# Optimization experiments

Hardware: AMD Instinct MI355X
Metric: run time of the kernel (lower is better)

The kernel has to match this reference:

```python
import jax, jax.numpy as jnp
import numpy as np

N = 100000      # nodes
E = 3200000     # edges (avg degree 32)
F_IN = 16       # data.num_features
H = 16          # hidden width (hard-coded in module)
C = 2           # data.num_classes
N_MID = 5       # conv2..conv6


def setup_inputs() -> dict:
    key = jax.random.key(0)
    ks = jax.random.split(key, 12)
    s = lambda fan_in: 1.0 / np.sqrt(fan_in)
    x = jax.random.normal(ks[0], (N, F_IN), jnp.float32)
    edge_index = jax.random.randint(ks[1], (2, E), 0, N, jnp.int32)
    return {
        "x": x,
        "edge_index": edge_index,
        "Wl1": jax.random.normal(ks[2], (F_IN, H), jnp.float32) * s(F_IN),
        "Wr1": jax.random.normal(ks[3], (F_IN, H), jnp.float32) * s(F_IN),
        "b1": jnp.zeros((H,), jnp.float32),
        "Wl_mid": jax.random.normal(ks[4], (N_MID, H, H), jnp.float32) * s(H),
        "Wr_mid": jax.random.normal(ks[5], (N_MID, H, H), jnp.float32) * s(H),
        "b_mid": jnp.zeros((N_MID, H), jnp.float32),
        "Wl7": jax.random.normal(ks[6], (H, C), jnp.float32) * s(H),
        "Wr7": jax.random.normal(ks[7], (H, C), jnp.float32) * s(H),
        "b7": jnp.zeros((C,), jnp.float32),
    }


def _sage_conv(x, src, dst, Wl, bl, Wr):
    # PyG SAGEConv(aggr='max'): out = lin_l(max_j x_j) + lin_r(x_i)
    msg = x[src]                                  # [E, F] neighbor gather
    agg = jax.ops.segment_max(msg, dst, num_segments=N)
    agg = jnp.where(jnp.isfinite(agg), agg, 0.0)  # isolated nodes -> 0
    return agg @ Wl + bl + x @ Wr


def reference(x, edge_index, Wl1, Wr1, b1, Wl_mid, Wr_mid, b_mid, Wl7, Wr7, b7):
    src, dst = edge_index[0], edge_index[1]
    h = jax.nn.relu(_sage_conv(x, src, dst, Wl1, b1, Wr1))
    for i in range(N_MID):
        h = jax.nn.relu(_sage_conv(h, src, dst, Wl_mid[i], b_mid[i], Wr_mid[i]))
    # F.dropout with training=False (inference) is identity
    h = _sage_conv(h, src, dst, Wl7, b7, Wr7)
    return jax.nn.log_softmax(h, axis=1)
```

## Files before the change

### kernel.cpp

```cpp
#include <hip/hip_runtime.h>
#include <hip/hip_fp16.h>

#define N_NODES 100000
#define N_EDGES 3200000
#define HDIM 16
#define NB 391
#define PAIRCAP 9216
#define COLCAP 13312
#define P1_THREADS 512
#define P1_EPB 4096
#define P1_BLOCKS ((N_EDGES + P1_EPB - 1) / P1_EPB)
#define SENT 0xFBFFFBFFu

typedef unsigned u32;

__device__ __forceinline__ u32 pkmax(u32 a, u32 b) {
    u32 r;
    asm("v_pk_max_f16 %0, %1, %2" : "=v"(r) : "v"(a), "v"(b));
    return r;
}
__device__ __forceinline__ float2 h2f2(u32 u) {
    __half2 h = *reinterpret_cast<__half2*>(&u);
    return __half22float2(h);
}
__device__ __forceinline__ u32 f2h2(float a, float b) {
    __half2 h = __float22half2_rn(make_float2(a, b));
    return *reinterpret_cast<u32*>(&h);
}


__global__ void f2h_zero(const float4* __restrict__ x, uint2* __restrict__ o, int n,
                         int* __restrict__ gcur) {
    int t = threadIdx.x;
    if (blockIdx.x == 0) {
        for (int k = t; k < NB; k += blockDim.x) gcur[k] = 0;
    }
    if (blockIdx.x == 1 && t < 8) {
        ((u32*)o)[(size_t)N_NODES * 8 + t] = SENT;
    }
    int i = blockIdx.x * blockDim.x + t;
    if (i < n) {
        float4 v = x[i];
        o[i] = make_uint2(f2h2(v.x, v.y), f2h2(v.z, v.w));
    }
}


__global__ __launch_bounds__(P1_THREADS)
void pass1_bucket(const int* __restrict__ src, const int* __restrict__ dst,
                  int* __restrict__ gcur, unsigned* __restrict__ pairs) {
    __shared__ int lh[NB], lbase[NB];
    int t = threadIdx.x;
    int e0 = blockIdx.x * P1_EPB;
    int n = min(P1_EPB, N_EDGES - e0);
    for (int i = t; i < NB; i += P1_THREADS) lh[i] = 0;
    __syncthreads();
    unsigned pv[8];
    int bk[8], rr[8];
#pragma unroll
    for (int k = 0; k < 8; ++k) {
        int idx = k * P1_THREADS + t;
        if (idx < n) {
            int d = dst[e0 + idx];
            int s = src[e0 + idx];
            bk[k] = d >> 8;
            pv[k] = (unsigned)s | ((unsigned)(d & 255) << 17);
            rr[k] = atomicAdd(&lh[bk[k]], 1);
        }
    }
    __syncthreads();
    for (int i = t; i < NB; i += P1_THREADS) {
        int c = lh[i];
        lbase[i] = c ? atomicAdd(&gcur[i], c) : 0;
    }
    __syncthreads();
#pragma unroll
    for (int k = 0; k < 8; ++k) {
        int idx = k * P1_THREADS + t;
        if (idx < n) {
            int p = lbase[bk[k]] + rr[k];
            if (p < PAIRCAP)
                pairs[(size_t)bk[k] * COLCAP + p] = pv[k];
        }
    }
}


__global__ __launch_bounds__(1024)
void pass2_sort(unsigned* __restrict__ colbuf, const int* __restrict__ gcur,
                int2* __restrict__ row2) {
    __shared__ int sdeg[256], spd[256], ssc[256];
    __shared__ int colst[COLCAP];
    __shared__ int stot;
    int t = threadIdx.x;
    int b = blockIdx.x;
    size_t base = (size_t)b * COLCAP;
    int cnt = min(gcur[b], PAIRCAP);
    int node0 = b << 8;
    int nn = min(256, N_NODES - node0);
    if (t < 256) sdeg[t] = 0;
    __syncthreads();
    unsigned vv[9];
    int rr[9];
#pragma unroll
    for (int k = 0; k < 9; ++k) {
        int j = k * 1024 + t;
        if (j < cnt) {
            unsigned v = colbuf[base + j];
            vv[k] = v;
            rr[k] = atomicAdd(&sdeg[v >> 17], 1);
        }
    }
    __syncthreads();
    if (t < 256) {
        int d = sdeg[t];
        int pd = (d + 15) & ~15;
        spd[t] = pd;
        ssc[t] = pd;
    }
    __syncthreads();
    for (int off = 1; off < 256; off <<= 1) {
        int u = 0;
        if (t < 256 && t >= off) u = ssc[t - off];
        __syncthreads();
        if (t < 256) ssc[t] += u;
        __syncthreads();
    }
    if (t < 256) {
        int ex = ssc[t] - spd[t];
        ssc[t] = ex;
        if (t < nn) row2[node0 + t] = make_int2((int)base + ex, (int)base + ex + spd[t]);
        if (t == 255) stot = ex + spd[t];
        for (int q = ex + sdeg[t]; q < ex + spd[t]; ++q)
            colst[q] = N_NODES;
    }
    __syncthreads();
#pragma unroll
    for (int k = 0; k < 9; ++k) {
        int j = k * 1024 + t;
        if (j < cnt) {
            unsigned v = vv[k];
            colst[ssc[v >> 17] + rr[k]] = v & 0x1FFFF;
        }
    }
    __syncthreads();
    int tot = stot;
    for (int j = t; j < tot; j += 1024) colbuf[base + j] = (unsigned)colst[j];
}


template <int HOUT, bool RELU, bool LSM>
__global__ void sage_layer(const u32* __restrict__ h,
                           const int2* __restrict__ row2,
                           const unsigned* __restrict__ col,
                           const float* __restrict__ Wl,
                           const float* __restrict__ Wr,
                           const float* __restrict__ b,
                           void* __restrict__ out) {
    __shared__ float sWl[HDIM * HOUT];
    __shared__ float sWr[HDIM * HOUT];
    __shared__ float sb[HOUT];
    int t = threadIdx.x;
    if (t < HDIM * HOUT) { sWl[t] = Wl[t]; sWr[t] = Wr[t]; }
    if (t < HOUT) sb[t] = b[t];
    if (HOUT == 16) {
        if (blockIdx.x == 0 && t < 8)
            ((u32*)out)[(size_t)N_NODES * 8 + t] = SENT;
    }
    __syncthreads();

    int nl = t >> 3, g = t & 7, p = g >> 1, hf = g & 1;
    int i = blockIdx.x * 32 + nl;
    if (i >= N_NODES) return;

    int2 r2 = row2[i];
    int beg = r2.x, endp = r2.y;
    const uint4* h4 = (const uint4*)h;

    u32 a0 = SENT, a1 = SENT, a2 = SENT, a3 = SENT;
    for (int j = beg; j < endp; j += 16) {
        int n0 = (int)col[j + p];
        int n1 = (int)col[j + 4 + p];
        int n2 = (int)col[j + 8 + p];
        int n3 = (int)col[j + 12 + p];
        uint4 v0 = h4[n0 * 2 + hf];
        uint4 v1 = h4[n1 * 2 + hf];
        uint4 v2 = h4[n2 * 2 + hf];
        uint4 v3 = h4[n3 * 2 + hf];
        a0 = pkmax(a0, pkmax(pkmax(v0.x, v1.x), pkmax(v2.x, v3.x)));
        a1 = pkmax(a1, pkmax(pkmax(v0.y, v1.y), pkmax(v2.y, v3.y)));
        a2 = pkmax(a2, pkmax(pkmax(v0.z, v1.z), pkmax(v2.z, v3.z)));
        a3 = pkmax(a3, pkmax(pkmax(v0.w, v1.w), pkmax(v2.w, v3.w)));
    }
#pragma unroll
    for (int m = 2; m <= 4; m <<= 1) {
        a0 = pkmax(a0, (u32)__shfl_xor((int)a0, m));
        a1 = pkmax(a1, (u32)__shfl_xor((int)a1, m));
        a2 = pkmax(a2, (u32)__shfl_xor((int)a2, m));
        a3 = pkmax(a3, (u32)__shfl_xor((int)a3, m));
    }
    if (beg == endp) { a0 = a1 = a2 = a3 = 0u; }

    uint4 xr = h4[i * 2 + hf];

    float fa[8], fx[8];
    {
        float2 f;
        f = h2f2(a0);   fa[0] = f.x; fa[1] = f.y;
        f = h2f2(a1);   fa[2] = f.x; fa[3] = f.y;
        f = h2f2(a2);   fa[4] = f.x; fa[5] = f.y;
        f = h2f2(a3);   fa[6] = f.x; fa[7] = f.y;
        f = h2f2(xr.x); fx[0] = f.x; fx[1] = f.y;
        f = h2f2(xr.y); fx[2] = f.x; fx[3] = f.y;
        f = h2f2(xr.z); fx[4] = f.x; fx[5] = f.y;
        f = h2f2(xr.w); fx[6] = f.x; fx[7] = f.y;
    }
    int fb = hf * 8;

    if (HOUT == 16) {
        float o0 = 0.f, o1 = 0.f, o2 = 0.f, o3 = 0.f;
#pragma unroll
        for (int q = 0; q < 8; ++q) {
            int f = fb + q;
            float4 wl = ((const float4*)sWl)[f * 4 + p];
            float4 wr = ((const float4*)sWr)[f * 4 + p];
            o0 += fa[q] * wl.x + fx[q] * wr.x;
            o1 += fa[q] * wl.y + fx[q] * wr.y;
            o2 += fa[q] * wl.z + fx[q] * wr.z;
            o3 += fa[q] * wl.w + fx[q] * wr.w;
        }
        o0 += __shfl_xor(o0, 1);
        o1 += __shfl_xor(o1, 1);
        o2 += __shfl_xor(o2, 1);
        o3 += __shfl_xor(o3, 1);
        if (hf == 0) {
            int c0 = p * 4;
            o0 += sb[c0]; o1 += sb[c0 + 1]; o2 += sb[c0 + 2]; o3 += sb[c0 + 3];
            if (RELU) {
                o0 = fmaxf(o0, 0.f); o1 = fmaxf(o1, 0.f);
                o2 = fmaxf(o2, 0.f); o3 = fmaxf(o3, 0.f);
            }
            ((uint2*)out)[i * 4 + p] = make_uint2(f2h2(o0, o1), f2h2(o2, o3));
        }
    } else {
        float o0 = 0.f, o1 = 0.f;
#pragma unroll
        for (int q = 0; q < 8; ++q) {
            int f = fb + q;
            o0 += fa[q] * sWl[f * 2 + 0] + fx[q] * sWr[f * 2 + 0];
            o1 += fa[q] * sWl[f * 2 + 1] + fx[q] * sWr[f * 2 + 1];
        }
        o0 += __shfl_xor(o0, 1);
        o1 += __shfl_xor(o1, 1);
        if (g == 0) {
            o0 += sb[0]; o1 += sb[1];
            if (LSM) {
                float m = fmaxf(o0, o1);
                float lse = m + logf(expf(o0 - m) + expf(o1 - m));
                o0 -= lse; o1 -= lse;
            }
            ((float2*)out)[i] = make_float2(o0, o1);
        }
    }
}


extern "C" void kernel_launch(void* const* d_in, const int* in_sizes, int n_in,
                              void* d_out, int out_size, void* d_ws, size_t ws_size,
                              hipStream_t stream) {
    const float* x      = (const float*)d_in[0];
    const int*   ei     = (const int*)d_in[1];
    const float* Wl1    = (const float*)d_in[2];
    const float* Wr1    = (const float*)d_in[3];
    const float* b1     = (const float*)d_in[4];
    const float* Wl_mid = (const float*)d_in[5];
    const float* Wr_mid = (const float*)d_in[6];
    const float* b_mid  = (const float*)d_in[7];
    const float* Wl7    = (const float*)d_in[8];
    const float* Wr7    = (const float*)d_in[9];
    const float* b7     = (const float*)d_in[10];
    float* out = (float*)d_out;

    const int* src = ei;
    const int* dst = ei + N_EDGES;

    char* ws = (char*)d_ws;
    size_t off = 0;
    auto alloc = [&](size_t bytes) {
        void* p = ws + off;
        off += (bytes + 255) & ~(size_t)255;
        return p;
    };
    unsigned* colbuf = (unsigned*)alloc((size_t)NB * COLCAP * 4);
    int2*    row2    = (int2*)alloc((size_t)N_NODES * 8);
    int*     gcur    = (int*)alloc((size_t)NB * 4);
    u32*     h0      = (u32*)alloc((size_t)(N_NODES + 1) * HDIM * 2);
    u32*     hA      = (u32*)alloc((size_t)(N_NODES + 1) * HDIM * 2);
    u32*     hB      = (u32*)alloc((size_t)(N_NODES + 1) * HDIM * 2);

    dim3 bL((N_NODES + 31) / 32);

    f2h_zero<<<(N_NODES * HDIM / 4 + 255) / 256, 256, 0, stream>>>(
        (const float4*)x, (uint2*)h0, N_NODES * HDIM / 4, gcur);
    pass1_bucket<<<P1_BLOCKS, P1_THREADS, 0, stream>>>(src, dst, gcur, colbuf);
    pass2_sort<<<NB, 1024, 0, stream>>>(colbuf, gcur, row2);

    sage_layer<16, true, false><<<bL, 256, 0, stream>>>(h0, row2, colbuf, Wl1, Wr1, b1, hA);

    u32* cur = hA;
    u32* nxt = hB;
    for (int i = 0; i < 5; ++i) {
        sage_layer<16, true, false><<<bL, 256, 0, stream>>>(
            cur, row2, colbuf, Wl_mid + i * 256, Wr_mid + i * 256, b_mid + i * 16, nxt);
        u32* tmp = cur; cur = nxt; nxt = tmp;
    }

    sage_layer<2, false, true><<<bL, 256, 0, stream>>>(cur, row2, colbuf, Wl7, Wr7, b7, out);
}
```

Baseline: 212.2 us.

## Vectorize and prefetch neighbor indices, fold fp16 conversion into bucketing pass

In each SAGE layer, every lane now loads its four neighbor indices with one 16-byte load. The next group of indices is prefetched during the current iteration, and the self-feature load is issued before the aggregation loop. The block barrier for the staged weights moves after the gather, so the gather no longer waits on it. The separate fp32-to-fp16 conversion kernel is removed: its work is folded into pass1_bucket, and the counter reset becomes a memset. A 16-entry sentinel pad is written after each bucket so the prefetch past the last row stays in bounds, and the node bounds check is dropped because the grid size divides the node count exactly.

```diff
diff --git a/kernel.cpp b/kernel.cpp
--- a/kernel.cpp
+++ b/kernel.cpp
@@ -29,28 +29,23 @@
 }
 
 
-__global__ void f2h_zero(const float4* __restrict__ x, uint2* __restrict__ o, int n,
-                         int* __restrict__ gcur) {
-    int t = threadIdx.x;
-    if (blockIdx.x == 0) {
-        for (int k = t; k < NB; k += blockDim.x) gcur[k] = 0;
-    }
-    if (blockIdx.x == 1 && t < 8) {
-        ((u32*)o)[(size_t)N_NODES * 8 + t] = SENT;
-    }
-    int i = blockIdx.x * blockDim.x + t;
-    if (i < n) {
-        float4 v = x[i];
-        o[i] = make_uint2(f2h2(v.x, v.y), f2h2(v.z, v.w));
-    }
-}
-
-
 __global__ __launch_bounds__(P1_THREADS)
 void pass1_bucket(const int* __restrict__ src, const int* __restrict__ dst,
-                  int* __restrict__ gcur, unsigned* __restrict__ pairs) {
+                  int* __restrict__ gcur, unsigned* __restrict__ pairs,
+                  const float4* __restrict__ x, uint2* __restrict__ h0) {
     __shared__ int lh[NB], lbase[NB];
     int t = threadIdx.x;
+
+    {
+        int ci = blockIdx.x * P1_THREADS + t;
+        if (ci < N_NODES * HDIM / 4) {
+            float4 v = x[ci];
+            h0[ci] = make_uint2(f2h2(v.x, v.y), f2h2(v.z, v.w));
+        }
+        if (blockIdx.x == 0 && t < 8)
+            ((u32*)h0)[(size_t)N_NODES * 8 + t] = SENT;
+    }
+
     int e0 = blockIdx.x * P1_EPB;
     int n = min(P1_EPB, N_EDGES - e0);
     for (int i = t; i < NB; i += P1_THREADS) lh[i] = 0;
@@ -146,6 +141,7 @@
     __syncthreads();
     int tot = stot;
     for (int j = t; j < tot; j += 1024) colbuf[base + j] = (unsigned)colst[j];
+    if (t < 16) colbuf[base + tot + t] = N_NODES;
 }
 
 
@@ -167,30 +163,31 @@
         if (blockIdx.x == 0 && t < 8)
             ((u32*)out)[(size_t)N_NODES * 8 + t] = SENT;
     }
-    __syncthreads();
 
     int nl = t >> 3, g = t & 7, p = g >> 1, hf = g & 1;
     int i = blockIdx.x * 32 + nl;
-    if (i >= N_NODES) return;
 
     int2 r2 = row2[i];
     int beg = r2.x, endp = r2.y;
     const uint4* h4 = (const uint4*)h;
 
+    uint4 xr = h4[i * 2 + hf];
+
     u32 a0 = SENT, a1 = SENT, a2 = SENT, a3 = SENT;
-    for (int j = beg; j < endp; j += 16) {
-        int n0 = (int)col[j + p];
-        int n1 = (int)col[j + 4 + p];
-        int n2 = (int)col[j + 8 + p];
-        int n3 = (int)col[j + 12 + p];
-        uint4 v0 = h4[n0 * 2 + hf];
-        uint4 v1 = h4[n1 * 2 + hf];
-        uint4 v2 = h4[n2 * 2 + hf];
-        uint4 v3 = h4[n3 * 2 + hf];
+    uint4 cc = *(const uint4*)(col + beg + 4 * p);
+    for (int j = beg; j < endp; ) {
+        int jn = j + 16;
+        uint4 nc = *(const uint4*)(col + jn + 4 * p);
+        uint4 v0 = h4[(int)cc.x * 2 + hf];
+        uint4 v1 = h4[(int)cc.y * 2 + hf];
+        uint4 v2 = h4[(int)cc.z * 2 + hf];
+        uint4 v3 = h4[(int)cc.w * 2 + hf];
         a0 = pkmax(a0, pkmax(pkmax(v0.x, v1.x), pkmax(v2.x, v3.x)));
         a1 = pkmax(a1, pkmax(pkmax(v0.y, v1.y), pkmax(v2.y, v3.y)));
         a2 = pkmax(a2, pkmax(pkmax(v0.z, v1.z), pkmax(v2.z, v3.z)));
         a3 = pkmax(a3, pkmax(pkmax(v0.w, v1.w), pkmax(v2.w, v3.w)));
+        cc = nc;
+        j = jn;
     }
 #pragma unroll
     for (int m = 2; m <= 4; m <<= 1) {
@@ -200,8 +197,6 @@
         a3 = pkmax(a3, (u32)__shfl_xor((int)a3, m));
     }
     if (beg == endp) { a0 = a1 = a2 = a3 = 0u; }
-
-    uint4 xr = h4[i * 2 + hf];
 
     float fa[8], fx[8];
     {
@@ -216,6 +211,8 @@
         f = h2f2(xr.w); fx[6] = f.x; fx[7] = f.y;
     }
     int fb = hf * 8;
+
+    __syncthreads();
 
     if (HOUT == 16) {
         float o0 = 0.f, o1 = 0.f, o2 = 0.f, o3 = 0.f;
@@ -300,9 +297,9 @@
 
     dim3 bL((N_NODES + 31) / 32);
 
-    f2h_zero<<<(N_NODES * HDIM / 4 + 255) / 256, 256, 0, stream>>>(
-        (const float4*)x, (uint2*)h0, N_NODES * HDIM / 4, gcur);
-    pass1_bucket<<<P1_BLOCKS, P1_THREADS, 0, stream>>>(src, dst, gcur, colbuf);
+    hipMemsetAsync(gcur, 0, NB * sizeof(int), stream);
+    pass1_bucket<<<P1_BLOCKS, P1_THREADS, 0, stream>>>(src, dst, gcur, colbuf,
+                                                       (const float4*)x, (uint2*)h0);
     pass2_sort<<<NB, 1024, 0, stream>>>(colbuf, gcur, row2);
 
     sage_layer<16, true, false><<<bL, 256, 0, stream>>>(h0, row2, colbuf, Wl1, Wr1, b1, hA);
```

After: 210.5 us. Within noise of the previous version (-0.8%).
